# Optimization experiments

Hardware: AMD Instinct MI355X
Metric: run time of the kernel (lower is better)

Reference implementation:

```python
import jax, jax.numpy as jnp
import numpy as np


def setup_inputs() -> dict:
    key = jax.random.key(0)
    ks = jax.random.split(key, 6)
    B, S, D, G, I, H = 4, 2048, 1024, 256, 1024, 16
    return {
        "inputs_embeds": jax.random.normal(ks[0], (B, S, D), dtype=jnp.float32),
        "structure_features": jax.random.normal(ks[1], (B, G), dtype=jnp.float32),
        "Wq": jax.random.normal(ks[2], (D, I), dtype=jnp.float32) * 0.02,
        "Wk": jax.random.normal(ks[3], (G, I), dtype=jnp.float32) * 0.02,
        "Wv": jax.random.normal(ks[4], (D, I), dtype=jnp.float32) * 0.02,
        "Wo": jax.random.normal(ks[5], (I, D), dtype=jnp.float32) * 0.02,
        "num_heads": 16,
    }


def reference(inputs_embeds, structure_features, Wq, Wk, Wv, Wo, num_heads):
    B, S, D = inputs_embeds.shape
    I = Wq.shape[1]
    H = num_heads
    hd = I // H
    scale = 1.0 / (hd ** 0.5)

    # queries/values from token embeddings: [B, S, I] -> [B, H, S, hd]
    q = (inputs_embeds @ Wq).reshape(B, S, H, hd).transpose(0, 2, 1, 3)
    v = (inputs_embeds @ Wv).reshape(B, S, H, hd).transpose(0, 2, 1, 3)

    # structure_features is repeat-expanded to seq_len in the original; the
    # projection of identical rows is identical, so project once and broadcast.
    k1 = (structure_features @ Wk).reshape(B, 1, H, hd).transpose(0, 2, 1, 3)  # [B, H, 1, hd]
    k = jnp.broadcast_to(k1, (B, H, S, hd))  # same values as key_proj(repeated sf)

    # [B, H, S, S] score matrix (columns identical by construction, as in the
    # original module) -> softmax -> weighted sum of values.
    scores = jnp.einsum("bhqd,bhkd->bhqk", q, k) * scale
    probs = jax.nn.softmax(scores, axis=-1)
    attended = jnp.einsum("bhqk,bhkd->bhqd", probs, v)  # [B, H, S, hd]

    attended = attended.transpose(0, 2, 1, 3).reshape(B, S, I)
    return attended @ Wo
```

## Files before the change

### kernel.cpp

```cpp
#include <hip/hip_runtime.h>

#define BB 4
#define SS 2048
#define DD 1024
#define II 1024


constexpr int CHUNK = 64;

__global__ void k_mean(const float* __restrict__ x, float* __restrict__ xbar) {
    const int b  = blockIdx.y;
    const int s0 = blockIdx.x * CHUNK;
    const int d4 = threadIdx.x;
    const float4* xr = (const float4*)(x + (size_t)b * SS * DD);
    float4 acc = make_float4(0.f, 0.f, 0.f, 0.f);
    #pragma unroll 4
    for (int r = 0; r < CHUNK; ++r) {
        float4 v = xr[(size_t)(s0 + r) * (DD / 4) + d4];
        acc.x += v.x; acc.y += v.y; acc.z += v.z; acc.w += v.w;
    }
    const float inv = 1.0f / (float)SS;
    float* dst = xbar + b * DD + d4 * 4;
    atomicAdd(dst + 0, acc.x * inv);
    atomicAdd(dst + 1, acc.y * inv);
    atomicAdd(dst + 2, acc.z * inv);
    atomicAdd(dst + 3, acc.w * inv);
}

constexpr int DCH = 128;

__global__ void k_gemv(const float* __restrict__ vin, const float* __restrict__ W,
                       float* __restrict__ vout, int K, int N) {
    const int i  = blockIdx.x * 256 + threadIdx.x;
    const int d0 = blockIdx.y * DCH;
    __shared__ float xs[BB][DCH];
    for (int idx = threadIdx.x; idx < BB * DCH; idx += 256) {
        int b = idx / DCH, d = idx % DCH;
        xs[b][d] = vin[b * K + d0 + d];
    }
    __syncthreads();
    float a0 = 0.f, a1 = 0.f, a2 = 0.f, a3 = 0.f;
    #pragma unroll 8
    for (int d = 0; d < DCH; ++d) {
        float w = W[(size_t)(d0 + d) * N + i];
        a0 += xs[0][d] * w;
        a1 += xs[1][d] * w;
        a2 += xs[2][d] * w;
        a3 += xs[3][d] * w;
    }
    atomicAdd(&vout[0 * N + i], a0);
    atomicAdd(&vout[1 * N + i], a1);
    atomicAdd(&vout[2 * N + i], a2);
    atomicAdd(&vout[3 * N + i], a3);
}

__global__ void k_bcast(const float* __restrict__ row, float4* __restrict__ out) {
    const size_t g = (size_t)blockIdx.x * blockDim.x + threadIdx.x;
    const int per_b = SS * (DD / 4);
    const int b  = (int)(g / per_b);
    const int d4 = (int)(g % (DD / 4));
    const float4* r = (const float4*)row;
    out[g] = r[b * (DD / 4) + d4];
}

extern "C" void kernel_launch(void* const* d_in, const int* in_sizes, int n_in,
                              void* d_out, int out_size, void* d_ws, size_t ws_size,
                              hipStream_t stream) {
    const float* x  = (const float*)d_in[0];
    const float* Wv = (const float*)d_in[4];
    const float* Wo = (const float*)d_in[5];
    float* out = (float*)d_out;

    float* xbar = (float*)d_ws;
    float* tbuf = xbar + BB * DD;
    float* orow = tbuf + BB * II;

    hipMemsetAsync(d_ws, 0, (size_t)(BB * DD + BB * II + BB * DD) * sizeof(float), stream);

    k_mean<<<dim3(SS / CHUNK, BB), 256, 0, stream>>>(x, xbar);
    k_gemv<<<dim3(II / 256, DD / DCH), 256, 0, stream>>>(xbar, Wv, tbuf, DD, II);
    k_gemv<<<dim3(DD / 256, II / DCH), 256, 0, stream>>>(tbuf, Wo, orow, II, DD);

    const size_t total4 = (size_t)BB * SS * DD / 4;
    k_bcast<<<(int)(total4 / 256), 256, 0, stream>>>(orow, (float4*)out);
}
```

Baseline: 125.7 us.

## Fuse mean, two GEMVs and broadcast into one cooperative kernel

Replaces the memset plus four separate launches (mean, two GEMVs, broadcast) with a single cooperative kernel of 512 blocks that uses grid-wide syncs between phases. The sequence mean is now computed as per-block partial sums written to a buffer and reduced in the GEMV phase, instead of many atomics into a shared vector. Workspace zeroing moves into the first phase. The goal is to remove launch and memset overhead and inter-kernel gaps. In exchange it adds three grid barriers and caps parallelism at 512 resident blocks for the memory-bound read and write phases.

```diff
diff --git a/kernel.cpp b/kernel.cpp
--- a/kernel.cpp
+++ b/kernel.cpp
@@ -1,4 +1,7 @@
 #include <hip/hip_runtime.h>
+#include <hip/hip_cooperative_groups.h>
+
+namespace cg = cooperative_groups;
 
 #define BB 4
 #define SS 2048
@@ -6,61 +9,112 @@
 #define II 1024
 
 
-constexpr int CHUNK = 64;
+constexpr int NBLK = 512;
+constexpr int NTHR = 256;
+constexpr int ROWS_PER_BLK = (BB * SS) / NBLK;
+constexpr int JCNT = SS / ROWS_PER_BLK;
+constexpr int KC = 32;
+constexpr int DCH = DD / KC;
 
-__global__ void k_mean(const float* __restrict__ x, float* __restrict__ xbar) {
-    const int b  = blockIdx.y;
-    const int s0 = blockIdx.x * CHUNK;
-    const int d4 = threadIdx.x;
-    const float4* xr = (const float4*)(x + (size_t)b * SS * DD);
-    float4 acc = make_float4(0.f, 0.f, 0.f, 0.f);
-    #pragma unroll 4
-    for (int r = 0; r < CHUNK; ++r) {
-        float4 v = xr[(size_t)(s0 + r) * (DD / 4) + d4];
-        acc.x += v.x; acc.y += v.y; acc.z += v.z; acc.w += v.w;
+__global__ __launch_bounds__(NTHR, 4)
+void fused_attention_collapse(const float* __restrict__ x,
+                              const float* __restrict__ Wv,
+                              const float* __restrict__ Wo,
+                              float* __restrict__ out,
+                              float* __restrict__ pbuf,
+                              float* __restrict__ tbuf,
+                              float* __restrict__ orow) {
+    cg::grid_group grid = cg::this_grid();
+    const int tid = threadIdx.x;
+    const int g   = blockIdx.x;
+
+    {
+        const int b = g / JCNT;
+        const int j = g % JCNT;
+        const float4* xr = (const float4*)(x + ((size_t)b * SS + (size_t)j * ROWS_PER_BLK) * DD);
+        float4 acc = make_float4(0.f, 0.f, 0.f, 0.f);
+        #pragma unroll
+        for (int r = 0; r < ROWS_PER_BLK; ++r) {
+            float4 v = xr[(size_t)r * (DD / 4) + tid];
+            acc.x += v.x; acc.y += v.y; acc.z += v.z; acc.w += v.w;
+        }
+        ((float4*)pbuf)[(size_t)g * (DD / 4) + tid] = acc;
+        if (tid < 16) tbuf[g * 16 + tid] = 0.f;
     }
-    const float inv = 1.0f / (float)SS;
-    float* dst = xbar + b * DD + d4 * 4;
-    atomicAdd(dst + 0, acc.x * inv);
-    atomicAdd(dst + 1, acc.y * inv);
-    atomicAdd(dst + 2, acc.z * inv);
-    atomicAdd(dst + 3, acc.w * inv);
-}
+    grid.sync();
 
-constexpr int DCH = 128;
+    __shared__ float xred[2][BB][DCH];
+    __shared__ float xs[BB][DCH];
+    if (g < KC * 4) {
+        const int kc = g >> 2, ic = g & 3;
+        const int d0 = kc * DCH;
+        const int half = tid >> 7;
+        const int e    = tid & 127;
+        const int b    = e / DCH, d = e % DCH;
+        float s = 0.f;
+        const int j0 = half * (JCNT / 2), j1 = j0 + (JCNT / 2);
+        #pragma unroll 8
+        for (int j = j0; j < j1; ++j)
+            s += pbuf[(size_t)(b * JCNT + j) * DD + d0 + d];
+        xred[half][b][d] = s;
+        __syncthreads();
+        if (tid < BB * DCH)
+            xs[b][d] = (xred[0][b][d] + xred[1][b][d]) * (1.0f / (float)SS);
+        __syncthreads();
 
-__global__ void k_gemv(const float* __restrict__ vin, const float* __restrict__ W,
-                       float* __restrict__ vout, int K, int N) {
-    const int i  = blockIdx.x * 256 + threadIdx.x;
-    const int d0 = blockIdx.y * DCH;
-    __shared__ float xs[BB][DCH];
-    for (int idx = threadIdx.x; idx < BB * DCH; idx += 256) {
-        int b = idx / DCH, d = idx % DCH;
-        xs[b][d] = vin[b * K + d0 + d];
+        const int i = ic * NTHR + tid;
+        float a0 = 0.f, a1 = 0.f, a2 = 0.f, a3 = 0.f;
+        #pragma unroll
+        for (int d2 = 0; d2 < DCH; ++d2) {
+            float w = Wv[(size_t)(d0 + d2) * II + i];
+            a0 += xs[0][d2] * w;
+            a1 += xs[1][d2] * w;
+            a2 += xs[2][d2] * w;
+            a3 += xs[3][d2] * w;
+        }
+        atomicAdd(&tbuf[0 * II + i], a0);
+        atomicAdd(&tbuf[1 * II + i], a1);
+        atomicAdd(&tbuf[2 * II + i], a2);
+        atomicAdd(&tbuf[3 * II + i], a3);
     }
-    __syncthreads();
-    float a0 = 0.f, a1 = 0.f, a2 = 0.f, a3 = 0.f;
-    #pragma unroll 8
-    for (int d = 0; d < DCH; ++d) {
-        float w = W[(size_t)(d0 + d) * N + i];
-        a0 += xs[0][d] * w;
-        a1 += xs[1][d] * w;
-        a2 += xs[2][d] * w;
-        a3 += xs[3][d] * w;
+    grid.sync();
+
+    __shared__ float ts[BB][DCH];
+    if (g < KC * 4) {
+        const int kc = g >> 2, ic = g & 3;
+        const int k0 = kc * DCH;
+        if (tid < BB * DCH) {
+            const int b = tid / DCH, kk = tid % DCH;
+            ts[b][kk] = tbuf[b * II + k0 + kk];
+        }
+        __syncthreads();
+        const int dcol = ic * NTHR + tid;
+        float a0 = 0.f, a1 = 0.f, a2 = 0.f, a3 = 0.f;
+        #pragma unroll
+        for (int kk = 0; kk < DCH; ++kk) {
+            float w = Wo[(size_t)(k0 + kk) * DD + dcol];
+            a0 += ts[0][kk] * w;
+            a1 += ts[1][kk] * w;
+            a2 += ts[2][kk] * w;
+            a3 += ts[3][kk] * w;
+        }
+        atomicAdd(&orow[0 * DD + dcol], a0);
+        atomicAdd(&orow[1 * DD + dcol], a1);
+        atomicAdd(&orow[2 * DD + dcol], a2);
+        atomicAdd(&orow[3 * DD + dcol], a3);
     }
-    atomicAdd(&vout[0 * N + i], a0);
-    atomicAdd(&vout[1 * N + i], a1);
-    atomicAdd(&vout[2 * N + i], a2);
-    atomicAdd(&vout[3 * N + i], a3);
-}
+    grid.sync();
 
-__global__ void k_bcast(const float* __restrict__ row, float4* __restrict__ out) {
-    const size_t g = (size_t)blockIdx.x * blockDim.x + threadIdx.x;
-    const int per_b = SS * (DD / 4);
-    const int b  = (int)(g / per_b);
-    const int d4 = (int)(g % (DD / 4));
-    const float4* r = (const float4*)row;
-    out[g] = r[b * (DD / 4) + d4];
+    {
+        const int b  = g / (NBLK / BB);
+        const int sg = g % (NBLK / BB);
+        const int s0 = sg * ROWS_PER_BLK;
+        float4 c = ((const float4*)orow)[b * (DD / 4) + tid];
+        float4* o4 = (float4*)out + ((size_t)b * SS + s0) * (DD / 4) + tid;
+        #pragma unroll
+        for (int r = 0; r < ROWS_PER_BLK; ++r)
+            o4[(size_t)r * (DD / 4)] = c;
+    }
 }
 
 extern "C" void kernel_launch(void* const* d_in, const int* in_sizes, int n_in,
@@ -71,16 +125,12 @@
     const float* Wo = (const float*)d_in[5];
     float* out = (float*)d_out;
 
-    float* xbar = (float*)d_ws;
-    float* tbuf = xbar + BB * DD;
-    float* orow = tbuf + BB * II;
+    float* pbuf = (float*)d_ws;
+    float* tbuf = pbuf + (size_t)NBLK * DD;
+    float* orow = tbuf + (size_t)BB * II;
 
-    hipMemsetAsync(d_ws, 0, (size_t)(BB * DD + BB * II + BB * DD) * sizeof(float), stream);
-
-    k_mean<<<dim3(SS / CHUNK, BB), 256, 0, stream>>>(x, xbar);
-    k_gemv<<<dim3(II / 256, DD / DCH), 256, 0, stream>>>(xbar, Wv, tbuf, DD, II);
-    k_gemv<<<dim3(DD / 256, II / DCH), 256, 0, stream>>>(tbuf, Wo, orow, II, DD);
-
-    const size_t total4 = (size_t)BB * SS * DD / 4;
-    k_bcast<<<(int)(total4 / 256), 256, 0, stream>>>(orow, (float4*)out);
+    void* args[] = { (void*)&x, (void*)&Wv, (void*)&Wo, (void*)&out,
+                     (void*)&pbuf, (void*)&tbuf, (void*)&orow };
+    hipLaunchCooperativeKernel((void*)fused_attention_collapse,
+                               dim3(NBLK), dim3(NTHR), args, 0, stream);
 }
```

New measurement: 281.1 us. +123.7%, slower.

## Replace atomics and memset with two-stage reduction and split-K GEMV

Applied to the files above, without the earlier changes.

The column mean is now computed by writing per-chunk partial sums to a workspace buffer, and the first GEMV reduces those partials, so no memset or atomic adds are needed. Each GEMV block now covers 16 output columns across the full K dimension and reduces the split-K partials in shared memory before a plain store. The broadcast kernel writes four rows per block, reusing one loaded row. This removes the memset launch and atomic contention, at the cost of redundant partial-sum reduction in every GEMV block and fewer GEMV blocks (64).

```diff
diff --git a/kernel.cpp b/kernel.cpp
--- a/kernel.cpp
+++ b/kernel.cpp
@@ -6,61 +6,72 @@
 #define II 1024
 
 
-constexpr int CHUNK = 64;
+constexpr int JP = 64;
+constexpr int ROWS1 = SS / JP;
 
-__global__ void k_mean(const float* __restrict__ x, float* __restrict__ xbar) {
-    const int b  = blockIdx.y;
-    const int s0 = blockIdx.x * CHUNK;
-    const int d4 = threadIdx.x;
-    const float4* xr = (const float4*)(x + (size_t)b * SS * DD);
-    float4 acc = make_float4(0.f, 0.f, 0.f, 0.f);
-    #pragma unroll 4
-    for (int r = 0; r < CHUNK; ++r) {
-        float4 v = xr[(size_t)(s0 + r) * (DD / 4) + d4];
-        acc.x += v.x; acc.y += v.y; acc.z += v.z; acc.w += v.w;
+__global__ __launch_bounds__(256)
+void k1_partial(const float* __restrict__ x, float4* __restrict__ pbuf) {
+    const int g = blockIdx.x;
+    const int b = g >> 6, j = g & 63;
+    const float4* xr = (const float4*)x + (size_t)(b * SS + j * ROWS1) * (DD / 4) + threadIdx.x;
+    float4 a = make_float4(0.f, 0.f, 0.f, 0.f);
+    #pragma unroll
+    for (int r = 0; r < ROWS1; ++r) {
+        float4 v = xr[(size_t)r * (DD / 4)];
+        a.x += v.x; a.y += v.y; a.z += v.z; a.w += v.w;
     }
-    const float inv = 1.0f / (float)SS;
-    float* dst = xbar + b * DD + d4 * 4;
-    atomicAdd(dst + 0, acc.x * inv);
-    atomicAdd(dst + 1, acc.y * inv);
-    atomicAdd(dst + 2, acc.z * inv);
-    atomicAdd(dst + 3, acc.w * inv);
+    pbuf[(size_t)g * (DD / 4) + threadIdx.x] = a;
 }
 
-constexpr int DCH = 128;
-
-__global__ void k_gemv(const float* __restrict__ vin, const float* __restrict__ W,
-                       float* __restrict__ vout, int K, int N) {
-    const int i  = blockIdx.x * 256 + threadIdx.x;
-    const int d0 = blockIdx.y * DCH;
-    __shared__ float xs[BB][DCH];
-    for (int idx = threadIdx.x; idx < BB * DCH; idx += 256) {
-        int b = idx / DCH, d = idx % DCH;
-        xs[b][d] = vin[b * K + d0 + d];
+__global__ __launch_bounds__(256)
+void k2_gemv(const float* __restrict__ vin, const float* __restrict__ W,
+             float* __restrict__ vout, int jp, float scale) {
+    __shared__ float xs[BB][DD];
+    const int tid = threadIdx.x;
+    for (int b = 0; b < BB; ++b) {
+        const float4* p = (const float4*)(vin + (size_t)b * jp * DD) + tid;
+        float4 a = make_float4(0.f, 0.f, 0.f, 0.f);
+        for (int j = 0; j < jp; ++j) {
+            float4 v = p[(size_t)j * (DD / 4)];
+            a.x += v.x; a.y += v.y; a.z += v.z; a.w += v.w;
+        }
+        ((float4*)xs[b])[tid] = make_float4(a.x * scale, a.y * scale, a.z * scale, a.w * scale);
     }
     __syncthreads();
-    float a0 = 0.f, a1 = 0.f, a2 = 0.f, a3 = 0.f;
+
+    const int i0 = blockIdx.x * 16;
+    const int il = tid & 15, ks = tid >> 4;
+    float acc[BB] = {0.f, 0.f, 0.f, 0.f};
     #pragma unroll 8
-    for (int d = 0; d < DCH; ++d) {
-        float w = W[(size_t)(d0 + d) * N + i];
-        a0 += xs[0][d] * w;
-        a1 += xs[1][d] * w;
-        a2 += xs[2][d] * w;
-        a3 += xs[3][d] * w;
+    for (int kk = 0; kk < 64; ++kk) {
+        const int k = ks * 64 + kk;
+        const float w = W[(size_t)k * 1024 + i0 + il];
+        #pragma unroll
+        for (int b = 0; b < BB; ++b) acc[b] += xs[b][k] * w;
     }
-    atomicAdd(&vout[0 * N + i], a0);
-    atomicAdd(&vout[1 * N + i], a1);
-    atomicAdd(&vout[2 * N + i], a2);
-    atomicAdd(&vout[3 * N + i], a3);
+
+    __shared__ float red[16][BB][16];
+    #pragma unroll
+    for (int b = 0; b < BB; ++b) red[ks][b][il] = acc[b];
+    __syncthreads();
+    if (tid < BB * 16) {
+        const int b = tid >> 4, i = tid & 15;
+        float s = 0.f;
+        #pragma unroll
+        for (int q = 0; q < 16; ++q) s += red[q][b][i];
+        vout[b * 1024 + i0 + i] = s;
+    }
 }
 
-__global__ void k_bcast(const float* __restrict__ row, float4* __restrict__ out) {
-    const size_t g = (size_t)blockIdx.x * blockDim.x + threadIdx.x;
-    const int per_b = SS * (DD / 4);
-    const int b  = (int)(g / per_b);
-    const int d4 = (int)(g % (DD / 4));
-    const float4* r = (const float4*)row;
-    out[g] = r[b * (DD / 4) + d4];
+__global__ __launch_bounds__(256)
+void k4_bcast(const float* __restrict__ orow, float4* __restrict__ out) {
+    const int g = blockIdx.x;
+    const int b = g >> 9;
+    const int s0 = (g & 511) * 4;
+    const float4 c = ((const float4*)(orow + b * DD))[threadIdx.x];
+    float4* o = out + (size_t)(b * SS + s0) * (DD / 4) + threadIdx.x;
+    #pragma unroll
+    for (int r = 0; r < 4; ++r) o[(size_t)r * (DD / 4)] = c;
 }
 
 extern "C" void kernel_launch(void* const* d_in, const int* in_sizes, int n_in,
@@ -71,16 +82,12 @@
     const float* Wo = (const float*)d_in[5];
     float* out = (float*)d_out;
 
-    float* xbar = (float*)d_ws;
-    float* tbuf = xbar + BB * DD;
-    float* orow = tbuf + BB * II;
+    float* pbuf = (float*)d_ws;
+    float* tvec = pbuf + (size_t)BB * JP * DD;
+    float* orow = tvec + (size_t)BB * II;
 
-    hipMemsetAsync(d_ws, 0, (size_t)(BB * DD + BB * II + BB * DD) * sizeof(float), stream);
-
-    k_mean<<<dim3(SS / CHUNK, BB), 256, 0, stream>>>(x, xbar);
-    k_gemv<<<dim3(II / 256, DD / DCH), 256, 0, stream>>>(xbar, Wv, tbuf, DD, II);
-    k_gemv<<<dim3(DD / 256, II / DCH), 256, 0, stream>>>(tbuf, Wo, orow, II, DD);
-
-    const size_t total4 = (size_t)BB * SS * DD / 4;
-    k_bcast<<<(int)(total4 / 256), 256, 0, stream>>>(orow, (float4*)out);
+    k1_partial<<<BB * JP, 256, 0, stream>>>(x, (float4*)pbuf);
+    k2_gemv<<<II / 16, 256, 0, stream>>>(pbuf, Wv, tvec, JP, 1.0f / (float)SS);
+    k2_gemv<<<DD / 16, 256, 0, stream>>>(tvec, Wo, orow, 1, 1.0f);
+    k4_bcast<<<(BB * SS) / 4, 256, 0, stream>>>(orow, (float4*)out);
 }
```

Measured after the change: 172.0 us. 36.9% more time.
